# Kernel optimization log

Measured on AMD Instinct MI355X. Metric: run time of the kernel, lower is better.

## Reference

```python
import jax, jax.numpy as jnp
import numpy as np

N = 50000      # total nodes
E = 800000     # total edges
IN = 8         # in_channels
H = 16         # hidden_dim
OUT = 16       # out_channels
B = 64         # number of graphs in batch


def _glorot(k, shape):
    fan_out, fan_in = shape[0], shape[1]
    lim = float(np.sqrt(6.0 / (fan_in + fan_out)))
    return jax.random.uniform(k, shape, jnp.float32, -lim, lim)


def setup_inputs() -> dict:
    key = jax.random.key(0)
    ks = jax.random.split(key, 12)
    return {
        "x": jax.random.normal(ks[0], (N, IN), jnp.float32),
        "edge_attr": jax.random.uniform(ks[1], (E, 1), jnp.float32),
        # edge MLP 1: Linear(1, H) -> ReLU -> Linear(H, IN*H)
        "W_e1a": _glorot(ks[2], (H, 1)), "b_e1a": jnp.zeros((H,), jnp.float32),
        "W_e1b": _glorot(ks[3], (IN * H, H)), "b_e1b": jnp.zeros((IN * H,), jnp.float32),
        "root1": _glorot(ks[4], (IN, H)), "bias1": jnp.zeros((H,), jnp.float32),
        # edge MLP 2: Linear(1, H) -> ReLU -> Linear(H, H*OUT)
        "W_e2a": _glorot(ks[5], (H, 1)), "b_e2a": jnp.zeros((H,), jnp.float32),
        "W_e2b": _glorot(ks[6], (H * OUT, H)), "b_e2b": jnp.zeros((H * OUT,), jnp.float32),
        "root2": _glorot(ks[7], (H, OUT)), "bias2": jnp.zeros((OUT,), jnp.float32),
        "edge_index": jax.random.randint(ks[8], (2, E), 0, N, jnp.int32),
        "batch": jnp.sort(jax.random.randint(ks[9], (N,), 0, B, jnp.int32)),
    }


def _segment_mean(vals, idx, num_segments):
    s = jax.ops.segment_sum(vals, idx, num_segments=num_segments)
    cnt = jax.ops.segment_sum(jnp.ones((vals.shape[0],), vals.dtype), idx,
                              num_segments=num_segments)
    return s / jnp.maximum(cnt, 1.0)[:, None]


def _nnconv(x, src, dst, edge_attr, Wa, ba, Wb, bb, root, bias, din, dout):
    # edge MLP -> per-edge weight matrix [E, din, dout]
    he = jax.nn.relu(edge_attr @ Wa.T + ba)
    We = (he @ Wb.T + bb).reshape(-1, din, dout)
    # per-edge matmul on gathered source features, scatter-mean to dst
    msg = jnp.einsum('ei,eio->eo', x[src], We)
    agg = _segment_mean(msg, dst, x.shape[0])
    return agg + x @ root + bias


def reference(x, edge_attr, W_e1a, b_e1a, W_e1b, b_e1b, root1, bias1,
              W_e2a, b_e2a, W_e2b, b_e2b, root2, bias2, edge_index, batch):
    src, dst = edge_index[0], edge_index[1]
    h = jax.nn.relu(_nnconv(x, src, dst, edge_attr,
                            W_e1a, b_e1a, W_e1b, b_e1b, root1, bias1, IN, H))
    h = jax.nn.relu(_nnconv(h, src, dst, edge_attr,
                            W_e2a, b_e2a, W_e2b, b_e2b, root2, bias2, H, OUT))
    g = _segment_mean(h, batch, B)  # global mean pool per graph
    return (h, g, batch)
```

## Files before the change

### kernel.cpp

```cpp
#include <hip/hip_runtime.h>
#include <hip/hip_bf16.h>

typedef __bf16 bf16;
typedef __bf16 bf16x8 __attribute__((ext_vector_type(8)));
typedef float  f32x4  __attribute__((ext_vector_type(4)));


__global__ void hist_deg(const int* __restrict__ eidx, int* __restrict__ deg, int E)
{
    int e = blockIdx.x * blockDim.x + threadIdx.x;
    if (e < E) atomicAdd(&deg[eidx[E + e]], 1);
}

__global__ void partial_sums(const int* __restrict__ deg, int* __restrict__ bsum, int N)
{
    __shared__ int ts[256];
    const int t = threadIdx.x;
    const int base = blockIdx.x * 1024 + t * 4;
    int s = 0;
#pragma unroll
    for (int k = 0; k < 4; ++k)
        if (base + k < N) s += deg[base + k];
    ts[t] = s;
    __syncthreads();
    for (int st = 128; st >= 1; st >>= 1) {
        if (t < st) ts[t] += ts[t + st];
        __syncthreads();
    }
    if (t == 0) bsum[blockIdx.x] = ts[0];
}

__global__ void scan_bsum(int* __restrict__ bsum, int nb)
{
    const int lane = threadIdx.x;
    int base = 0;
    for (int start = 0; start < nb; start += 64) {
        int i = start + lane;
        int orig = (i < nb) ? bsum[i] : 0;
        int v = orig;
        for (int off = 1; off < 64; off <<= 1) {
            int u = __shfl_up(v, off, 64);
            if (lane >= off) v += u;
        }
        if (i < nb) bsum[i] = base + v - orig;
        base += __shfl(v, 63, 64);
    }
}

__global__ void emit_cursor(const int* __restrict__ deg, const int* __restrict__ bsum,
                            int* __restrict__ cursor, int N)
{
    __shared__ int ts[256];
    const int t = threadIdx.x;
    const int base = blockIdx.x * 1024 + t * 4;
    int v[4];
#pragma unroll
    for (int k = 0; k < 4; ++k)
        v[k] = (base + k < N) ? deg[base + k] : 0;
    int s = v[0] + v[1] + v[2] + v[3];
    ts[t] = s;
    __syncthreads();
    for (int off = 1; off < 256; off <<= 1) {
        int add = (t >= off) ? ts[t - off] : 0;
        __syncthreads();
        ts[t] += add;
        __syncthreads();
    }
    int excl = ts[t] - s + bsum[blockIdx.x];
    if (base + 0 < N) cursor[base + 0] = excl;
    if (base + 1 < N) cursor[base + 1] = excl + v[0];
    if (base + 2 < N) cursor[base + 2] = excl + v[0] + v[1];
    if (base + 3 < N) cursor[base + 3] = excl + v[0] + v[1] + v[2];
}

__global__ void scatter_edges(const int* __restrict__ eidx, const float* __restrict__ ea,
                              int* __restrict__ cursor,
                              int* __restrict__ src_s, int* __restrict__ dst_s,
                              float* __restrict__ ea_s, int E)
{
    int e = blockIdx.x * blockDim.x + threadIdx.x;
    if (e >= E) return;
    int d = eidx[E + e];
    int p = atomicAdd(&cursor[d], 1);
    src_s[p] = eidx[e];
    dst_s[p] = d;
    ea_s[p]  = ea[e];
}

__global__ void node_pre1(const float* __restrict__ x,
                          const float* __restrict__ root1,
                          const float* __restrict__ bias1,
                          float* __restrict__ r1, int N)
{
    int t = blockIdx.x * blockDim.x + threadIdx.x;
    int v = t >> 4, o = t & 15;
    if (v >= N) return;
    float racc = 0.f;
#pragma unroll
    for (int i = 0; i < 8; ++i)
        racc += x[v * 8 + i] * root1[i * 16 + o];
    r1[v * 16 + o] = racc + bias1[o];
}

__global__ void edge_l1(const float* __restrict__ x,
                        const float* __restrict__ ea_s,
                        const int*   __restrict__ src_s, const int* __restrict__ dst_s,
                        const float* __restrict__ W_e1a, const float* __restrict__ b_e1a,
                        const float* __restrict__ W_e1b, const float* __restrict__ b_e1b,
                        float* __restrict__ agg, int ntiles)
{
    const int lane = threadIdx.x & 63;
    const int m = lane & 15;
    const int q = lane >> 4;
    const int wave   = blockIdx.x * (blockDim.x >> 6) + (threadIdx.x >> 6);
    const int nwaves = gridDim.x * (blockDim.x >> 6);

    bf16x8 bfrag[4];
#pragma unroll
    for (int c = 0; c < 4; ++c)
#pragma unroll
        for (int t = 0; t < 8; ++t)
            bfrag[c][t] = (bf16)W_e1b[(t * 16 + m) * 16 + (c * 4 + q)];
    bf16x8 bfrag5 = {};
    if (q == 0)
#pragma unroll
        for (int t = 0; t < 8; ++t)
            bfrag5[t] = (bf16)b_e1b[t * 16 + m];

    for (int tile = wave; tile < ntiles; tile += nwaves) {
        int e = tile * 16 + m;
        int s = src_s[e];
        int d = dst_s[e];
        float t_ea = ea_s[e];

        float he[4];
#pragma unroll
        for (int c = 0; c < 4; ++c) {
            int j = c * 4 + q;
            float h = W_e1a[j] * t_ea + b_e1a[j];
            he[c] = h > 0.f ? h : 0.f;
        }

        const float4* xp = (const float4*)(x + (size_t)s * 8);
        float4 x0 = xp[0], x1 = xp[1];
        float xv[8] = {x0.x, x0.y, x0.z, x0.w, x1.x, x1.y, x1.z, x1.w};

        f32x4 acc = {0.f, 0.f, 0.f, 0.f};
#pragma unroll
        for (int c = 0; c < 4; ++c) {
            bf16x8 afrag;
#pragma unroll
            for (int t = 0; t < 8; ++t) afrag[t] = (bf16)(he[c] * xv[t]);
            acc = __builtin_amdgcn_mfma_f32_16x16x32_bf16(afrag, bfrag[c], acc, 0, 0, 0);
        }
        {
            bf16x8 a5 = {};
            if (q == 0)
#pragma unroll
                for (int t = 0; t < 8; ++t) a5[t] = (bf16)xv[t];
            acc = __builtin_amdgcn_mfma_f32_16x16x32_bf16(a5, bfrag5, acc, 0, 0, 0);
        }

        int   run_d   = __shfl(d, 0, 64);
        float run_sum = 0.f;
#pragma unroll
        for (int r = 0; r < 16; ++r) {
            int   dr = __shfl(d, r, 64);
            float vr = __shfl(acc[r & 3], ((r >> 2) << 4) + m, 64);
            if (dr != run_d) {
                if (q == 0) atomicAdd(&agg[(size_t)run_d * 16 + m], run_sum);
                run_sum = 0.f; run_d = dr;
            }
            run_sum += vr;
        }
        if (q == 0) atomicAdd(&agg[(size_t)run_d * 16 + m], run_sum);
    }
}

__global__ void node_fin1(const float* __restrict__ agg, const int* __restrict__ deg,
                          const float* __restrict__ r1,
                          const float* __restrict__ root2,
                          const float* __restrict__ bias2,
                          float* __restrict__ h1, float* __restrict__ r2, int N)
{
    int t = blockIdx.x * blockDim.x + threadIdx.x;
    int v = t >> 4, o = t & 15;
    if (v >= N) return;
    float c = (float)deg[v]; c = c > 1.f ? c : 1.f;
    float h = agg[v * 16 + o] / c + r1[v * 16 + o];
    h = h > 0.f ? h : 0.f;
    h1[v * 16 + o] = h;
    float racc = 0.f;
#pragma unroll
    for (int i = 0; i < 16; ++i)
        racc += __shfl(h, i, 16) * root2[i * 16 + o];
    r2[v * 16 + o] = racc + bias2[o];
}

__global__ void edge_l2(const float* __restrict__ h1g,
                        const float* __restrict__ ea_s,
                        const int*   __restrict__ src_s, const int* __restrict__ dst_s,
                        const float* __restrict__ W_e2a, const float* __restrict__ b_e2a,
                        const float* __restrict__ W_e2b, const float* __restrict__ b_e2b,
                        float* __restrict__ agg, int ntiles)
{
    const int lane = threadIdx.x & 63;
    const int m = lane & 15;
    const int q = lane >> 4;
    const int qh = q >> 1;
    const int ql = q & 1;
    const int wave   = blockIdx.x * (blockDim.x >> 6) + (threadIdx.x >> 6);
    const int nwaves = gridDim.x * (blockDim.x >> 6);

    bf16x8 bfrag[8];
#pragma unroll
    for (int c = 0; c < 8; ++c) {
        int j = c * 2 + qh;
#pragma unroll
        for (int t = 0; t < 8; ++t)
            bfrag[c][t] = (bf16)W_e2b[((ql * 8 + t) * 16 + m) * 16 + j];
    }
    bf16x8 bfrag5 = {};
    if (q < 2)
#pragma unroll
        for (int t = 0; t < 8; ++t)
            bfrag5[t] = (bf16)b_e2b[(q * 8 + t) * 16 + m];

    for (int tile = wave; tile < ntiles; tile += nwaves) {
        int e = tile * 16 + m;
        int s = src_s[e];
        int d = dst_s[e];
        float t_ea = ea_s[e];

        float he[8];
#pragma unroll
        for (int c = 0; c < 8; ++c) {
            int j = c * 2 + qh;
            float h = W_e2a[j] * t_ea + b_e2a[j];
            he[c] = h > 0.f ? h : 0.f;
        }

        const float4* hp = (const float4*)(h1g + (size_t)s * 16 + ql * 8);
        float4 h0 = hp[0], h1v = hp[1];
        float hv[8] = {h0.x, h0.y, h0.z, h0.w, h1v.x, h1v.y, h1v.z, h1v.w};

        f32x4 acc = {0.f, 0.f, 0.f, 0.f};
#pragma unroll
        for (int c = 0; c < 8; ++c) {
            bf16x8 afrag;
#pragma unroll
            for (int t = 0; t < 8; ++t) afrag[t] = (bf16)(he[c] * hv[t]);
            acc = __builtin_amdgcn_mfma_f32_16x16x32_bf16(afrag, bfrag[c], acc, 0, 0, 0);
        }
        {
            bf16x8 a5 = {};
            if (q < 2)
#pragma unroll
                for (int t = 0; t < 8; ++t) a5[t] = (bf16)hv[t];
            acc = __builtin_amdgcn_mfma_f32_16x16x32_bf16(a5, bfrag5, acc, 0, 0, 0);
        }

        int   run_d   = __shfl(d, 0, 64);
        float run_sum = 0.f;
#pragma unroll
        for (int r = 0; r < 16; ++r) {
            int   dr = __shfl(d, r, 64);
            float vr = __shfl(acc[r & 3], ((r >> 2) << 4) + m, 64);
            if (dr != run_d) {
                if (q == 0) atomicAdd(&agg[(size_t)run_d * 16 + m], run_sum);
                run_sum = 0.f; run_d = dr;
            }
            run_sum += vr;
        }
        if (q == 0) atomicAdd(&agg[(size_t)run_d * 16 + m], run_sum);
    }
}

__global__ void node_fin2(const float* __restrict__ agg, const int* __restrict__ deg,
                          const float* __restrict__ r2, const int* __restrict__ batch,
                          float* __restrict__ out_h, float* __restrict__ out_b, int N)
{
    int t = blockIdx.x * blockDim.x + threadIdx.x;
    int v = t >> 4, o = t & 15;
    if (v >= N) return;
    float c = (float)deg[v]; c = c > 1.f ? c : 1.f;
    float h = agg[v * 16 + o] / c + r2[v * 16 + o];
    h = h > 0.f ? h : 0.f;
    out_h[v * 16 + o] = h;
    if (o == 0) out_b[v] = (float)batch[v];
}

__global__ void pool_seg(const float* __restrict__ h, const int* __restrict__ batch,
                         float* __restrict__ out_g, int N)
{
    const int b = blockIdx.x;
    int lo = 0, hi = N;
    while (lo < hi) { int mid = (lo + hi) >> 1; if (batch[mid] < b) lo = mid + 1; else hi = mid; }
    const int start = lo;
    hi = N;
    while (lo < hi) { int mid = (lo + hi) >> 1; if (batch[mid] < b + 1) lo = mid + 1; else hi = mid; }
    const int end = lo;

    const int ch = threadIdx.x & 15, grp = threadIdx.x >> 4;
    float acc = 0.f;
    for (int v = start + grp; v < end; v += 16)
        acc += h[(size_t)v * 16 + ch];

    __shared__ float red[256];
    red[threadIdx.x] = acc;
    __syncthreads();
#pragma unroll
    for (int s = 128; s >= 16; s >>= 1) {
        if (threadIdx.x < s) red[threadIdx.x] += red[threadIdx.x + s];
        __syncthreads();
    }
    if (threadIdx.x < 16) {
        float c = (float)(end - start); c = c > 1.f ? c : 1.f;
        out_g[b * 16 + threadIdx.x] = red[threadIdx.x] / c;
    }
}

extern "C" void kernel_launch(void* const* d_in, const int* in_sizes, int n_in,
                              void* d_out, int out_size, void* d_ws, size_t ws_size,
                              hipStream_t stream)
{
    const float* x     = (const float*)d_in[0];
    const float* ea    = (const float*)d_in[1];
    const float* W_e1a = (const float*)d_in[2];
    const float* b_e1a = (const float*)d_in[3];
    const float* W_e1b = (const float*)d_in[4];
    const float* b_e1b = (const float*)d_in[5];
    const float* root1 = (const float*)d_in[6];
    const float* bias1 = (const float*)d_in[7];
    const float* W_e2a = (const float*)d_in[8];
    const float* b_e2a = (const float*)d_in[9];
    const float* W_e2b = (const float*)d_in[10];
    const float* b_e2b = (const float*)d_in[11];
    const float* root2 = (const float*)d_in[12];
    const float* bias2 = (const float*)d_in[13];
    const int*   eidx  = (const int*)d_in[14];
    const int*   batch = (const int*)d_in[15];

    const int E  = in_sizes[1];
    const int N  = in_sizes[15];
    const int Bg = (out_size - N * 16 - N) / 16;

    char* ws = (char*)d_ws;
    size_t off = 0;
    int*   deg  = (int*)(ws + off);   off += (size_t)N * 4;
    float* agg1 = (float*)(ws + off); off += (size_t)N * 16 * 4;
    float* agg2 = (float*)(ws + off); off += (size_t)N * 16 * 4;
    size_t zero_bytes = off;
    int*   bsum   = (int*)(ws + off); off += 1024 * 4;
    int*   cursor = (int*)(ws + off); off += (size_t)N * 4;
    int*   src_s  = (int*)(ws + off); off += (size_t)E * 4;
    int*   dst_s  = (int*)(ws + off); off += (size_t)E * 4;
    float* ea_s   = (float*)(ws + off); off += (size_t)E * 4;
    float* h1 = (float*)(ws + off); off += (size_t)N * 16 * 4;
    float* r1 = (float*)(ws + off); off += (size_t)N * 16 * 4;
    float* r2 = (float*)(ws + off); off += (size_t)N * 16 * 4;

    hipMemsetAsync(d_ws, 0, zero_bytes, stream);

    int nodeBlocks = (N * 16 + 255) / 256;
    int edgeBlocks = (E + 255) / 256;
    int scanBlocks = (N + 1023) / 1024;
    int ntiles = E / 16;

    hist_deg<<<edgeBlocks, 256, 0, stream>>>(eidx, deg, E);
    partial_sums<<<scanBlocks, 256, 0, stream>>>(deg, bsum, N);
    scan_bsum<<<1, 64, 0, stream>>>(bsum, scanBlocks);
    emit_cursor<<<scanBlocks, 256, 0, stream>>>(deg, bsum, cursor, N);
    scatter_edges<<<edgeBlocks, 256, 0, stream>>>(eidx, ea, cursor,
                                                  src_s, dst_s, ea_s, E);

    node_pre1<<<nodeBlocks, 256, 0, stream>>>(x, root1, bias1, r1, N);
    edge_l1<<<2048, 256, 0, stream>>>(x, ea_s, src_s, dst_s,
                                      W_e1a, b_e1a, W_e1b, b_e1b, agg1, ntiles);
    node_fin1<<<nodeBlocks, 256, 0, stream>>>(agg1, deg, r1, root2, bias2,
                                              h1, r2, N);
    edge_l2<<<2048, 256, 0, stream>>>(h1, ea_s, src_s, dst_s,
                                      W_e2a, b_e2a, W_e2b, b_e2b, agg2, ntiles);

    float* out_h = (float*)d_out;
    float* out_g = out_h + (size_t)N * 16;
    float* out_b = out_g + (size_t)Bg * 16;
    node_fin2<<<nodeBlocks, 256, 0, stream>>>(agg2, deg, r2, batch, out_h,
                                              out_b, N);
    pool_seg<<<Bg, 256, 0, stream>>>(out_h, batch, out_g, N);
}
```

Before: 348.6 us.

## Commit edge-tile scatter via per-lane run merging and two-tile unrolled loop

Replaces the 16-step serial shuffle/run-length reduction, in which only a quarter of lanes issue atomics, with each lane merging its own four accumulator rows by destination and issuing atomics directly. This removes around 32 shuffles per tile at the cost of potentially more atomic operations, since runs that cross quad boundaries are no longer merged. The first-layer edge MLP weights are hoisted out of the loop, the tile loop is unrolled by two to expose more memory-level parallelism, and the grid shrinks from 2048 to 1280 blocks.

```diff
diff --git a/kernel.cpp b/kernel.cpp
--- a/kernel.cpp
+++ b/kernel.cpp
@@ -102,6 +102,22 @@
     r1[v * 16 + o] = racc + bias1[o];
 }
 
+__device__ __forceinline__ void commit_runs(const f32x4& acc, const int* rd,
+                                            float* __restrict__ agg, int m)
+{
+    float run = acc[0];
+    int   cur = rd[0];
+#pragma unroll
+    for (int k = 1; k < 4; ++k) {
+        if (rd[k] == cur) run += acc[k];
+        else {
+            atomicAdd(&agg[(size_t)cur * 16 + m], run);
+            cur = rd[k]; run = acc[k];
+        }
+    }
+    atomicAdd(&agg[(size_t)cur * 16 + m], run);
+}
+
 __global__ void edge_l1(const float* __restrict__ x,
                         const float* __restrict__ ea_s,
                         const int*   __restrict__ src_s, const int* __restrict__ dst_s,
@@ -127,53 +143,51 @@
         for (int t = 0; t < 8; ++t)
             bfrag5[t] = (bf16)b_e1b[t * 16 + m];
 
-    for (int tile = wave; tile < ntiles; tile += nwaves) {
-        int e = tile * 16 + m;
-        int s = src_s[e];
-        int d = dst_s[e];
-        float t_ea = ea_s[e];
-
-        float he[4];
-#pragma unroll
-        for (int c = 0; c < 4; ++c) {
-            int j = c * 4 + q;
-            float h = W_e1a[j] * t_ea + b_e1a[j];
-            he[c] = h > 0.f ? h : 0.f;
+    const float wa[4] = { W_e1a[q], W_e1a[4 + q], W_e1a[8 + q], W_e1a[12 + q] };
+    const float ba[4] = { b_e1a[q], b_e1a[4 + q], b_e1a[8 + q], b_e1a[12 + q] };
+
+    for (int base = wave * 2; base < ntiles; base += nwaves * 2) {
+#pragma unroll
+        for (int u = 0; u < 2; ++u) {
+            int tile = base + u;
+            if (tile >= ntiles) break;
+            int e = tile * 16 + m;
+            int s = src_s[e];
+            int d = dst_s[e];
+            float t_ea = ea_s[e];
+
+            float he[4];
+#pragma unroll
+            for (int c = 0; c < 4; ++c) {
+                float h = wa[c] * t_ea + ba[c];
+                he[c] = h > 0.f ? h : 0.f;
+            }
+
+            const float4* xp = (const float4*)(x + (size_t)s * 8);
+            float4 x0 = xp[0], x1 = xp[1];
+            float xv[8] = {x0.x, x0.y, x0.z, x0.w, x1.x, x1.y, x1.z, x1.w};
+
+            f32x4 acc = {0.f, 0.f, 0.f, 0.f};
+#pragma unroll
+            for (int c = 0; c < 4; ++c) {
+                bf16x8 afrag;
+#pragma unroll
+                for (int t = 0; t < 8; ++t) afrag[t] = (bf16)(he[c] * xv[t]);
+                acc = __builtin_amdgcn_mfma_f32_16x16x32_bf16(afrag, bfrag[c], acc, 0, 0, 0);
+            }
+            {
+                bf16x8 a5 = {};
+                if (q == 0)
+#pragma unroll
+                    for (int t = 0; t < 8; ++t) a5[t] = (bf16)xv[t];
+                acc = __builtin_amdgcn_mfma_f32_16x16x32_bf16(a5, bfrag5, acc, 0, 0, 0);
+            }
+
+            int rd[4];
+#pragma unroll
+            for (int k = 0; k < 4; ++k) rd[k] = __shfl(d, 4 * q + k, 64);
+            commit_runs(acc, rd, agg, m);
         }
-
-        const float4* xp = (const float4*)(x + (size_t)s * 8);
-        float4 x0 = xp[0], x1 = xp[1];
-        float xv[8] = {x0.x, x0.y, x0.z, x0.w, x1.x, x1.y, x1.z, x1.w};
-
-        f32x4 acc = {0.f, 0.f, 0.f, 0.f};
-#pragma unroll
-        for (int c = 0; c < 4; ++c) {
-            bf16x8 afrag;
-#pragma unroll
-            for (int t = 0; t < 8; ++t) afrag[t] = (bf16)(he[c] * xv[t]);
-            acc = __builtin_amdgcn_mfma_f32_16x16x32_bf16(afrag, bfrag[c], acc, 0, 0, 0);
-        }
-        {
-            bf16x8 a5 = {};
-            if (q == 0)
-#pragma unroll
-                for (int t = 0; t < 8; ++t) a5[t] = (bf16)xv[t];
-            acc = __builtin_amdgcn_mfma_f32_16x16x32_bf16(a5, bfrag5, acc, 0, 0, 0);
-        }
-
-        int   run_d   = __shfl(d, 0, 64);
-        float run_sum = 0.f;
-#pragma unroll
-        for (int r = 0; r < 16; ++r) {
-            int   dr = __shfl(d, r, 64);
-            float vr = __shfl(acc[r & 3], ((r >> 2) << 4) + m, 64);
-            if (dr != run_d) {
-                if (q == 0) atomicAdd(&agg[(size_t)run_d * 16 + m], run_sum);
-                run_sum = 0.f; run_d = dr;
-            }
-            run_sum += vr;
-        }
-        if (q == 0) atomicAdd(&agg[(size_t)run_d * 16 + m], run_sum);
     }
 }
 
@@ -226,53 +240,55 @@
         for (int t = 0; t < 8; ++t)
             bfrag5[t] = (bf16)b_e2b[(q * 8 + t) * 16 + m];
 
-    for (int tile = wave; tile < ntiles; tile += nwaves) {
-        int e = tile * 16 + m;
-        int s = src_s[e];
-        int d = dst_s[e];
-        float t_ea = ea_s[e];
-
-        float he[8];
-#pragma unroll
-        for (int c = 0; c < 8; ++c) {
-            int j = c * 2 + qh;
-            float h = W_e2a[j] * t_ea + b_e2a[j];
-            he[c] = h > 0.f ? h : 0.f;
+    float wa[8], ba[8];
+#pragma unroll
+    for (int c = 0; c < 8; ++c) {
+        wa[c] = W_e2a[c * 2 + qh];
+        ba[c] = b_e2a[c * 2 + qh];
+    }
+
+    for (int base = wave * 2; base < ntiles; base += nwaves * 2) {
+#pragma unroll
+        for (int u = 0; u < 2; ++u) {
+            int tile = base + u;
+            if (tile >= ntiles) break;
+            int e = tile * 16 + m;
+            int s = src_s[e];
+            int d = dst_s[e];
+            float t_ea = ea_s[e];
+
+            float he[8];
+#pragma unroll
+            for (int c = 0; c < 8; ++c) {
+                float h = wa[c] * t_ea + ba[c];
+                he[c] = h > 0.f ? h : 0.f;
+            }
+
+            const float4* hp = (const float4*)(h1g + (size_t)s * 16 + ql * 8);
+            float4 h0 = hp[0], h1v = hp[1];
+            float hv[8] = {h0.x, h0.y, h0.z, h0.w, h1v.x, h1v.y, h1v.z, h1v.w};
+
+            f32x4 acc = {0.f, 0.f, 0.f, 0.f};
+#pragma unroll
+            for (int c = 0; c < 8; ++c) {
+                bf16x8 afrag;
+#pragma unroll
+                for (int t = 0; t < 8; ++t) afrag[t] = (bf16)(he[c] * hv[t]);
+                acc = __builtin_amdgcn_mfma_f32_16x16x32_bf16(afrag, bfrag[c], acc, 0, 0, 0);
+            }
+            {
+                bf16x8 a5 = {};
+                if (q < 2)
+#pragma unroll
+                    for (int t = 0; t < 8; ++t) a5[t] = (bf16)hv[t];
+                acc = __builtin_amdgcn_mfma_f32_16x16x32_bf16(a5, bfrag5, acc, 0, 0, 0);
+            }
+
+            int rd[4];
+#pragma unroll
+            for (int k = 0; k < 4; ++k) rd[k] = __shfl(d, 4 * q + k, 64);
+            commit_runs(acc, rd, agg, m);
         }
-
-        const float4* hp = (const float4*)(h1g + (size_t)s * 16 + ql * 8);
-        float4 h0 = hp[0], h1v = hp[1];
-        float hv[8] = {h0.x, h0.y, h0.z, h0.w, h1v.x, h1v.y, h1v.z, h1v.w};
-
-        f32x4 acc = {0.f, 0.f, 0.f, 0.f};
-#pragma unroll
-        for (int c = 0; c < 8; ++c) {
-            bf16x8 afrag;
-#pragma unroll
-            for (int t = 0; t < 8; ++t) afrag[t] = (bf16)(he[c] * hv[t]);
-            acc = __builtin_amdgcn_mfma_f32_16x16x32_bf16(afrag, bfrag[c], acc, 0, 0, 0);
-        }
-        {
-            bf16x8 a5 = {};
-            if (q < 2)
-#pragma unroll
-                for (int t = 0; t < 8; ++t) a5[t] = (bf16)hv[t];
-            acc = __builtin_amdgcn_mfma_f32_16x16x32_bf16(a5, bfrag5, acc, 0, 0, 0);
-        }
-
-        int   run_d   = __shfl(d, 0, 64);
-        float run_sum = 0.f;
-#pragma unroll
-        for (int r = 0; r < 16; ++r) {
-            int   dr = __shfl(d, r, 64);
-            float vr = __shfl(acc[r & 3], ((r >> 2) << 4) + m, 64);
-            if (dr != run_d) {
-                if (q == 0) atomicAdd(&agg[(size_t)run_d * 16 + m], run_sum);
-                run_sum = 0.f; run_d = dr;
-            }
-            run_sum += vr;
-        }
-        if (q == 0) atomicAdd(&agg[(size_t)run_d * 16 + m], run_sum);
     }
 }
 
@@ -375,11 +391,11 @@
                                                   src_s, dst_s, ea_s, E);
 
     node_pre1<<<nodeBlocks, 256, 0, stream>>>(x, root1, bias1, r1, N);
-    edge_l1<<<2048, 256, 0, stream>>>(x, ea_s, src_s, dst_s,
+    edge_l1<<<1280, 256, 0, stream>>>(x, ea_s, src_s, dst_s,
                                       W_e1a, b_e1a, W_e1b, b_e1b, agg1, ntiles);
     node_fin1<<<nodeBlocks, 256, 0, stream>>>(agg1, deg, r1, root2, bias2,
                                               h1, r2, N);
-    edge_l2<<<2048, 256, 0, stream>>>(h1, ea_s, src_s, dst_s,
+    edge_l2<<<1280, 256, 0, stream>>>(h1, ea_s, src_s, dst_s,
                                       W_e2a, b_e2a, W_e2b, b_e2b, agg2, ntiles);
 
     float* out_h = (float*)d_out;
```

Result: faster. 329.4 us (-5.5%).
